# Performance work log

Measured on AMD Instinct MI355X. Metric: run time of the kernel, lower is better.

## Reference

```python
import jax, jax.numpy as jnp
import numpy as np

B, S, N, BS, D, H, V = 1, 2048, 128, 16, 512, 8, 32000
MASK_TOKEN_ID = 3


def setup_inputs() -> dict:
    key = jax.random.key(0)
    ks = jax.random.split(key, 10)
    anchors = jnp.sort(jax.random.randint(ks[0], (B, N), 0, S - BS), axis=1)
    return {
        "input_ids": jax.random.randint(ks[1], (B, S), 0, V),
        "hidden_states": jax.random.normal(ks[2], (B, S, D), dtype=jnp.float32),
        "loss_mask": jnp.ones((B, S), dtype=jnp.float32),
        "anchor_positions": anchors,
        "block_keep_mask": jnp.ones((B, N), dtype=bool),
        "embed_table": jax.random.normal(ks[3], (V, D), dtype=jnp.float32) * 0.02,
        "Wq": jax.random.normal(ks[4], (D, D), dtype=jnp.float32) * 0.02,
        "Wk": jax.random.normal(ks[5], (D, D), dtype=jnp.float32) * 0.02,
        "Wv": jax.random.normal(ks[6], (D, D), dtype=jnp.float32) * 0.02,
        "Wo": jax.random.normal(ks[7], (D, D), dtype=jnp.float32) * 0.02,
        "W_lm": jax.random.normal(ks[8], (D, V), dtype=jnp.float32) * 0.02,
    }


def dflash_sdpa_mask(anchor_positions, block_keep_mask):
    # KV layout: [context S | block_0 .. block_{N-1}], Q layout: [block_0 .. block_{N-1}]
    Q = N * BS
    KV = S + N * BS
    q_idx = jnp.arange(Q)              # [Q]
    kv_idx = jnp.arange(KV)            # [KV]
    q_blk = q_idx // BS                # [Q]
    anchor_q = anchor_positions[:, q_blk]          # [B,Q] anchor of each query's block
    keep_q = block_keep_mask[:, q_blk]             # [B,Q]
    is_ctx = kv_idx < S                             # [KV]
    mask_context = is_ctx[None, None, :] & (kv_idx[None, None, :] < anchor_q[:, :, None])  # [B,Q,KV]
    kv_blk = (kv_idx - S) // BS
    mask_draft = (kv_idx >= S)[None, :] & (q_blk[:, None] == kv_blk[None, :])              # [Q,KV]
    final = (mask_context | mask_draft[None]) & keep_q[:, :, None]                          # [B,Q,KV]
    return final


def reference(input_ids, hidden_states, loss_mask, anchor_positions, block_keep_mask,
              embed_table, Wq, Wk, Wv, Wo, W_lm):
    dh = D // H
    Q = N * BS

    # --- noise embedding: MASK token everywhere, anchor token at each block start ---
    safe_anchor = jnp.clip(anchor_positions, 0, S - 1)                     # [B,N]
    anchor_tokens = jnp.take_along_axis(input_ids, safe_anchor, axis=1)    # [B,N]
    start_tokens = jnp.where(block_keep_mask, anchor_tokens, MASK_TOKEN_ID)
    noise_ids = jnp.full((B, Q), MASK_TOKEN_ID, dtype=input_ids.dtype)
    noise_ids = noise_ids.at[:, jnp.arange(N) * BS].set(start_tokens)
    noise_embedding = embed_table[noise_ids]                               # [B,Q,D]

    # --- draft attention: Q = draft tokens, KV = [context hiddens | draft tokens] ---
    kv_in = jnp.concatenate([hidden_states, noise_embedding], axis=1)      # [B,S+Q,D]
    q = (noise_embedding @ Wq).reshape(B, Q, H, dh)
    k = (kv_in @ Wk).reshape(B, S + Q, H, dh)
    v = (kv_in @ Wv).reshape(B, S + Q, H, dh)
    scores = jnp.einsum("bqhd,bkhd->bhqk", q, k) / jnp.sqrt(jnp.float32(dh))
    mask = dflash_sdpa_mask(anchor_positions, block_keep_mask)[:, None]    # [B,1,Q,KV]
    attn = jax.nn.softmax(jnp.where(mask, scores, -1e9), axis=-1)
    out = jnp.einsum("bhqk,bkhd->bqhd", attn, v).reshape(B, Q, D) @ Wo     # [B,Q,D]
    logits = out @ W_lm                                                    # [B,Q,V]

    # --- block-wise CE loss ---
    offs = jnp.arange(BS)
    label_idx = anchor_positions[:, :, None] + offs[None, None, :]         # [B,N,BS]
    valid_label = label_idx < S
    safe_idx = jnp.clip(label_idx, 0, S - 1)
    ids_b = jnp.broadcast_to(input_ids[:, None, :], (B, N, S))
    target_ids = jnp.take_along_axis(ids_b, safe_idx, axis=2)              # [B,N,BS]
    lm_b = jnp.broadcast_to(loss_mask[:, None, :], (B, N, S))
    lm_g = jnp.take_along_axis(lm_b, safe_idx, axis=2)
    weight = (block_keep_mask[:, :, None].astype(jnp.float32)
              * valid_label.astype(jnp.float32)
              * (offs > 0)[None, None, :].astype(jnp.float32)
              * lm_g)                                                      # [B,N,BS]

    flat_logits = logits.reshape(-1, V)
    flat_targets = target_ids.reshape(-1)
    flat_w = weight.reshape(-1)
    logp = jax.nn.log_softmax(flat_logits, axis=-1)
    loss_per = -jnp.take_along_axis(logp, flat_targets[:, None], axis=1)[:, 0]
    loss = jnp.sum(loss_per * flat_w) / (jnp.sum(flat_w) + 1e-6)

    pred = jnp.argmax(flat_logits, axis=-1)
    correct = (pred == flat_targets) & (flat_w > 0.5)
    accuracy = jnp.sum(correct).astype(jnp.float32) / (jnp.sum(flat_w) + 1e-6)
    return loss, accuracy
```

## Files before the change

### kernel.cpp

```cpp
#include <hip/hip_runtime.h>

typedef unsigned short u16;
typedef __attribute__((ext_vector_type(4))) float f32x4;
typedef __attribute__((ext_vector_type(8))) short short8;
typedef __attribute__((ext_vector_type(4))) unsigned int uv4;
typedef __attribute__((ext_vector_type(4))) float fv4;
typedef __attribute__((ext_vector_type(4))) unsigned short usv4;

#define S_LEN 2048
#define NBLK 128
#define DMODEL 512
#define VOCAB 32000
#define QLEN 2048
#define KVLEN 4096
#define NSPLIT 250

#define GAS(p) ((const __attribute__((address_space(1))) void*)(const void*)(p))
#define LAS(p) ((__attribute__((address_space(3))) void*)(void*)(p))

__device__ __forceinline__ float bf2f(u16 u){
  union { unsigned int i; float f; } x; x.i = ((unsigned int)u) << 16; return x.f;
}
__device__ __forceinline__ u16 f2bf(float f){
  union { float f; unsigned int i; } x; x.f = f;
  unsigned int r = x.i + 0x7fffu + ((x.i >> 16) & 1u);
  return (u16)(r >> 16);
}

__global__ __launch_bounds__(256) void prep_w(const float* __restrict__ Wq, const float* __restrict__ Wk,
                                              const float* __restrict__ Wv, const float* __restrict__ Wo,
                                              const float* __restrict__ Wlm,
                                              u16* __restrict__ WqT, u16* __restrict__ WkT,
                                              u16* __restrict__ WvT, u16* __restrict__ WoT,
                                              u16* __restrict__ Wf){
  __shared__ float tile[64][33];
  int t = threadIdx.x;
  int id = blockIdx.x;
  if (id < 1024){
    const float* in; u16* out;
    switch (id >> 8){
      case 0: in = Wq; out = WqT; break;
      case 1: in = Wk; out = WkT; break;
      case 2: in = Wv; out = WvT; break;
      default: in = Wo; out = WoT; break;
    }
    int rem = id & 255;
    int nb = (rem & 15) * 32, kb = (rem >> 4) * 32;
    int tx = t & 31, ty = t >> 5;
    #pragma unroll
    for (int i = 0; i < 4; i++){
      int r = ty + i * 8;
      tile[r][tx] = in[(size_t)(kb + r) * 512 + nb + tx];
    }
    __syncthreads();
    #pragma unroll
    for (int i = 0; i < 4; i++){
      int r = ty + i * 8;
      out[(size_t)(nb + r) * 512 + kb + tx] = f2bf(tile[tx][r]);
    }
  } else {
    int j = id - 1024;
    int vb32 = j % 1000, kblk = j / 1000;
    int tx = t & 31, ty = t >> 5;
    #pragma unroll
    for (int i = 0; i < 8; i++){
      int r = ty + i * 8;
      tile[r][tx] = Wlm[(size_t)(kblk * 64 + r) * VOCAB + vb32 * 32 + tx];
    }
    __syncthreads();
    int w = t >> 6, lane = t & 63;
    int v16sel = w & 1, ktsel = w >> 1;
    int gsel = lane >> 4, li = lane & 15;
    u16 tmp[8];
    #pragma unroll
    for (int jj = 0; jj < 8; jj++)
      tmp[jj] = f2bf(tile[ktsel * 32 + gsel * 8 + jj][v16sel * 16 + li]);
    size_t v16 = vb32 * 2 + v16sel;
    size_t kt32 = kblk * 2 + ktsel;
    *(uv4*)&Wf[((v16 * 16 + kt32) * 64 + lane) * 8] = *(uv4*)tmp;
  }
}

__global__ __launch_bounds__(128) void build_kv(const float* __restrict__ hidden,
                                                const float* __restrict__ embed,
                                                const int* __restrict__ input_ids,
                                                const int* __restrict__ anchors,
                                                const unsigned char* __restrict__ keep,
                                                u16* __restrict__ kvb){
  int row = blockIdx.x;
  int t = threadIdx.x;
  const float* src;
  if (row < S_LEN){
    src = hidden + (size_t)row * DMODEL;
  } else {
    int q = row - S_LEN;
    int id = 3;
    if ((q & 15) == 0){
      int n = q >> 4;
      if (keep[n]){
        int a = anchors[n]; a = min(max(a, 0), S_LEN - 1);
        id = input_ids[a];
      }
    }
    src = embed + (size_t)id * DMODEL;
  }
  int c = t * 4;
  fv4 v = *(const fv4*)&src[c];
  usv4 o; o[0] = f2bf(v[0]); o[1] = f2bf(v[1]); o[2] = f2bf(v[2]); o[3] = f2bf(v[3]);
  *(usv4*)&kvb[(size_t)row * DMODEL + c] = o;
}

__global__ __launch_bounds__(256) void qkv_gemm(const u16* __restrict__ kvb,
                                                const u16* __restrict__ WkT,
                                                const u16* __restrict__ WvT,
                                                const u16* __restrict__ WqT,
                                                u16* __restrict__ kb,
                                                u16* __restrict__ vTb,
                                                u16* __restrict__ qb2){
  __shared__ __align__(16) u16 As[2][128 * 64];
  __shared__ __align__(16) u16 Bs[2][64 * 64];
  int id = blockIdx.x;
  const u16* A = kvb; const u16* BT; u16* C; int ldc; int trans = 0;
  int rowbase, colbase;
  if (id < 256){
    BT = WkT; C = kb; ldc = 512;
    rowbase = (id & 31) * 128; colbase = (id >> 5) * 64;
  } else if (id < 512){
    int j = id - 256;
    BT = WvT; C = vTb; ldc = KVLEN; trans = 1;
    rowbase = (j & 31) * 128; colbase = (j >> 5) * 64;
  } else {
    int j = id - 512;
    A = kvb + (size_t)S_LEN * DMODEL;
    BT = WqT; C = qb2; ldc = 512;
    rowbase = (j & 15) * 128; colbase = (j >> 4) * 64;
  }
  int t = threadIdx.x, w = t >> 6, lane = t & 63;
  int g = lane >> 4, li = lane & 15;
  int r0 = t >> 3, cg0 = t & 7;
  int swz = (cg0 ^ (r0 & 7)) << 3;

  auto stageA = [&](u16* dst, int kb_){
    #pragma unroll
    for (int i = 0; i < 4; i++)
      __builtin_amdgcn_global_load_lds(GAS(&A[(size_t)(rowbase + r0 + i * 32) * DMODEL + kb_ + swz]),
                                       LAS(dst + i * 2048 + w * 512), 16, 0, 0);
  };
  auto stageB = [&](u16* dst, int kb_){
    #pragma unroll
    for (int i = 0; i < 2; i++)
      __builtin_amdgcn_global_load_lds(GAS(&BT[(size_t)(colbase + r0 + i * 32) * DMODEL + kb_ + swz]),
                                       LAS(dst + i * 2048 + w * 512), 16, 0, 0);
  };

  f32x4 acc[2][4];
  #pragma unroll
  for (int i = 0; i < 2; i++)
    #pragma unroll
    for (int j = 0; j < 4; j++)
      acc[i][j] = (f32x4){0.f, 0.f, 0.f, 0.f};

  stageA(As[0], 0); stageB(Bs[0], 0);

  for (int kt = 0; kt < 8; kt++){
    u16* curA = As[kt & 1]; u16* curB = Bs[kt & 1];
    if (kt < 7){
      stageA(As[(kt + 1) & 1], (kt + 1) * 64); stageB(Bs[(kt + 1) & 1], (kt + 1) * 64);
      asm volatile("s_waitcnt vmcnt(6)" ::: "memory");
    } else {
      asm volatile("s_waitcnt vmcnt(0)" ::: "memory");
    }
    __builtin_amdgcn_s_barrier();
    #pragma unroll
    for (int ks = 0; ks < 2; ks++){
      short8 af[2], bf[4];
      #pragma unroll
      for (int mf = 0; mf < 2; mf++){
        int row = w * 32 + mf * 16 + li;
        af[mf] = *(const short8*)&curA[row * 64 + (((ks * 4 + g) ^ (li & 7)) << 3)];
      }
      #pragma unroll
      for (int nf = 0; nf < 4; nf++){
        int row = nf * 16 + li;
        bf[nf] = *(const short8*)&curB[row * 64 + (((ks * 4 + g) ^ (li & 7)) << 3)];
      }
      #pragma unroll
      for (int mf = 0; mf < 2; mf++)
        #pragma unroll
        for (int nf = 0; nf < 4; nf++)
          acc[mf][nf] = __builtin_amdgcn_mfma_f32_16x16x32_bf16(af[mf], bf[nf], acc[mf][nf], 0, 0, 0);
    }
    __builtin_amdgcn_s_barrier();
  }

  #pragma unroll
  for (int mf = 0; mf < 2; mf++)
    #pragma unroll
    for (int nf = 0; nf < 4; nf++)
      #pragma unroll
      for (int r = 0; r < 4; r++){
        int row = rowbase + w * 32 + mf * 16 + g * 4 + r;
        int col = colbase + nf * 16 + li;
        u16 vv = f2bf(acc[mf][nf][r]);
        if (trans) C[(size_t)col * ldc + row] = vv;
        else       C[(size_t)row * ldc + col] = vv;
      }
}

__global__ __launch_bounds__(256) void gemmO(const u16* __restrict__ A,
                                             const u16* __restrict__ BT,
                                             u16* __restrict__ C){
  __shared__ __align__(16) u16 As[2][128 * 64];
  __shared__ __align__(16) u16 Bs[2][64 * 64];
  int t = threadIdx.x, w = t >> 6, lane = t & 63;
  int g = lane >> 4, li = lane & 15;
  int rowbase = blockIdx.x * 128, colbase = blockIdx.y * 64;
  int r0 = t >> 3, cg0 = t & 7;
  int swz = (cg0 ^ (r0 & 7)) << 3;

  auto stageA = [&](u16* dst, int kb_){
    #pragma unroll
    for (int i = 0; i < 4; i++)
      __builtin_amdgcn_global_load_lds(GAS(&A[(size_t)(rowbase + r0 + i * 32) * DMODEL + kb_ + swz]),
                                       LAS(dst + i * 2048 + w * 512), 16, 0, 0);
  };
  auto stageB = [&](u16* dst, int kb_){
    #pragma unroll
    for (int i = 0; i < 2; i++)
      __builtin_amdgcn_global_load_lds(GAS(&BT[(size_t)(colbase + r0 + i * 32) * DMODEL + kb_ + swz]),
                                       LAS(dst + i * 2048 + w * 512), 16, 0, 0);
  };

  f32x4 acc[2][4];
  #pragma unroll
  for (int i = 0; i < 2; i++)
    #pragma unroll
    for (int j = 0; j < 4; j++)
      acc[i][j] = (f32x4){0.f, 0.f, 0.f, 0.f};

  stageA(As[0], 0); stageB(Bs[0], 0);

  for (int kt = 0; kt < 8; kt++){
    u16* curA = As[kt & 1]; u16* curB = Bs[kt & 1];
    if (kt < 7){
      stageA(As[(kt + 1) & 1], (kt + 1) * 64); stageB(Bs[(kt + 1) & 1], (kt + 1) * 64);
      asm volatile("s_waitcnt vmcnt(6)" ::: "memory");
    } else {
      asm volatile("s_waitcnt vmcnt(0)" ::: "memory");
    }
    __builtin_amdgcn_s_barrier();
    #pragma unroll
    for (int ks = 0; ks < 2; ks++){
      short8 af[2], bf[4];
      #pragma unroll
      for (int mf = 0; mf < 2; mf++){
        int row = w * 32 + mf * 16 + li;
        af[mf] = *(const short8*)&curA[row * 64 + (((ks * 4 + g) ^ (li & 7)) << 3)];
      }
      #pragma unroll
      for (int nf = 0; nf < 4; nf++){
        int row = nf * 16 + li;
        bf[nf] = *(const short8*)&curB[row * 64 + (((ks * 4 + g) ^ (li & 7)) << 3)];
      }
      #pragma unroll
      for (int mf = 0; mf < 2; mf++)
        #pragma unroll
        for (int nf = 0; nf < 4; nf++)
          acc[mf][nf] = __builtin_amdgcn_mfma_f32_16x16x32_bf16(af[mf], bf[nf], acc[mf][nf], 0, 0, 0);
    }
    __builtin_amdgcn_s_barrier();
  }

  #pragma unroll
  for (int mf = 0; mf < 2; mf++)
    #pragma unroll
    for (int nf = 0; nf < 4; nf++)
      #pragma unroll
      for (int r = 0; r < 4; r++){
        int row = rowbase + w * 32 + mf * 16 + g * 4 + r;
        int col = colbase + nf * 16 + li;
        C[(size_t)row * DMODEL + col] = f2bf(acc[mf][nf][r]);
      }
}

__global__ __launch_bounds__(256) void attn_mfma(const u16* __restrict__ qb,
                                                 const u16* __restrict__ kb,
                                                 const u16* __restrict__ vT,
                                                 const int* __restrict__ anchors,
                                                 const unsigned char* __restrict__ keep,
                                                 u16* __restrict__ attnb){
  int bx = blockIdx.x;
  int n = (bx & 1) ? (NBLK - 1 - (bx >> 1)) : (bx >> 1);
  int h = blockIdx.y;
  int t = threadIdx.x, w = t >> 6, lane = t & 63;
  int g = lane >> 4, li = lane & 15;

  __shared__ __align__(16) u16 q_s[16][72];
  __shared__ __align__(16) u16 p_s[4][16][72];
  __shared__ float o_s[4][16][64];
  __shared__ float l_s[4][16];

  {
    int r = t >> 4, c4 = (t & 15) * 4;
    usv4 v = *(const usv4*)&qb[(size_t)(n * 16 + r) * DMODEL + h * 64 + c4];
    usv4 o;
    #pragma unroll
    for (int j = 0; j < 4; j++) o[j] = f2bf(bf2f(v[j]) * 0.125f);
    *(usv4*)&q_s[r][c4] = o;
  }
  __syncthreads();

  int anchor = anchors[n];
  bool kp = keep[n] != 0;
  const u16* kh  = kb + h * 64;
  const u16* vTh = vT + (size_t)(h * 64) * KVLEN;

  if (!kp){
    if (w == 0){
      float acc = 0.f;
      const u16* row = vTh + (size_t)lane * KVLEN;
      for (int k2 = 0; k2 < KVLEN; k2 += 8){
        short8 vv = *(const short8*)&row[k2];
        #pragma unroll
        for (int j = 0; j < 8; j++) acc += bf2f((u16)vv[j]);
      }
      acc *= (1.f / 4096.f);
      u16 ov = f2bf(acc);
      for (int r = 0; r < 16; r++)
        attnb[(size_t)(n * 16 + r) * DMODEL + h * 64 + lane] = ov;
    }
    return;
  }

  short8 qa[2];
  #pragma unroll
  for (int ks = 0; ks < 2; ks++)
    qa[ks] = *(const short8*)&q_s[li][ks * 32 + g * 8];

  int nctx = (anchor + 63) >> 6;
  int ntot = nctx + 1;

  f32x4 o_acc[4];
  float l[4];
  #pragma unroll
  for (int i = 0; i < 4; i++){ o_acc[i] = (f32x4){0.f,0.f,0.f,0.f}; l[i] = 0.f; }

  for (int c = w; c < ntot; c += 4){
    bool draft = (c == nctx);
    int kbase = draft ? (S_LEN + n * 16) : c * 64;
    int nk    = draft ? 16 : min(64, anchor - c * 64);

    f32x4 s[4];
    #pragma unroll
    for (int nf = 0; nf < 4; nf++) s[nf] = (f32x4){0.f,0.f,0.f,0.f};
    #pragma unroll
    for (int ks = 0; ks < 2; ks++){
      #pragma unroll
      for (int nf = 0; nf < 4; nf++){
        int krow = min(kbase + nf * 16 + li, KVLEN - 1);
        short8 bfrag = *(const short8*)&kh[(size_t)krow * DMODEL + ks * 32 + g * 8];
        s[nf] = __builtin_amdgcn_mfma_f32_16x16x32_bf16(qa[ks], bfrag, s[nf], 0, 0, 0);
      }
    }

    #pragma unroll
    for (int r = 0; r < 4; r++){
      float ps = 0.f;
      #pragma unroll
      for (int nf = 0; nf < 4; nf++){
        float p = (nf * 16 + li < nk) ? __expf(s[nf][r]) : 0.f;
        ps += p;
        p_s[w][g * 4 + r][nf * 16 + li] = f2bf(p);
      }
      #pragma unroll
      for (int mm = 1; mm < 16; mm <<= 1) ps += __shfl_xor(ps, mm);
      l[r] += ps;
    }

    #pragma unroll
    for (int ks = 0; ks < 2; ks++){
      short8 pa = *(const short8*)&p_s[w][li][ks * 32 + g * 8];
      int kcol = min(kbase + ks * 32 + g * 8, KVLEN - 8);
      #pragma unroll
      for (int nfd = 0; nfd < 4; nfd++){
        short8 vfrag = *(const short8*)&vTh[(size_t)(nfd * 16 + li) * KVLEN + kcol];
        o_acc[nfd] = __builtin_amdgcn_mfma_f32_16x16x32_bf16(pa, vfrag, o_acc[nfd], 0, 0, 0);
      }
    }
  }

  #pragma unroll
  for (int r = 0; r < 4; r++){
    if (li == 0) l_s[w][g * 4 + r] = l[r];
    #pragma unroll
    for (int nfd = 0; nfd < 4; nfd++)
      o_s[w][g * 4 + r][nfd * 16 + li] = o_acc[nfd][r];
  }
  __syncthreads();

  {
    int row = t >> 4, c0 = (t & 15) * 4;
    float L = l_s[0][row] + l_s[1][row] + l_s[2][row] + l_s[3][row];
    float inv = 1.f / L;
    #pragma unroll
    for (int j = 0; j < 4; j++){
      float ov = o_s[0][row][c0 + j] + o_s[1][row][c0 + j] + o_s[2][row][c0 + j] + o_s[3][row][c0 + j];
      attnb[(size_t)(n * 16 + row) * DMODEL + h * 64 + c0 + j] = f2bf(ov * inv);
    }
  }
}

__global__ __launch_bounds__(256) void lm_fused(const u16* __restrict__ obp,
                                                const u16* __restrict__ Wf,
                                                const int* __restrict__ input_ids,
                                                const int* __restrict__ anchors,
                                                float* __restrict__ pl,
                                                float* __restrict__ pt, float* __restrict__ pbv,
                                                int* __restrict__ pbi){
  __shared__ __align__(16) u16 Ob[2][128 * 64];
  __shared__ int tcol_s[128];

  int L = blockIdx.x;
  int T = (L & 7) * 500 + (L >> 3);
  int qbase = (T & 15) * 128;
  int vb = T >> 4;
  int vocabbase = vb * 128;
  int t = threadIdx.x, w = t >> 6, lane = t & 63;
  int g = lane >> 4, li = lane & 15;
  int wv = w & 1, wq = w >> 1;

  if (t < 128){
    int r = qbase + t; int n = r >> 4, off = r & 15;
    int lab = anchors[n] + off;
    int safe = min(max(lab, 0), S_LEN - 1);
    tcol_s[t] = input_ids[safe];
  }

  int r0 = t >> 3, cg0 = t & 7;
  int swz = (cg0 ^ (r0 & 7)) << 3;
  auto stageO = [&](u16* odst, int kt){
    #pragma unroll
    for (int i = 0; i < 4; i++)
      __builtin_amdgcn_global_load_lds(GAS(&obp[(size_t)(qbase + r0 + i * 32) * DMODEL + kt * 64 + swz]),
                                       LAS(odst + i * 2048 + w * 512), 16, 0, 0);
  };
  const u16* wbase = Wf + ((size_t)(vb * 8 + wv * 4) * 16) * 512 + lane * 8;

  f32x4 acc[4][4];
  #pragma unroll
  for (int i = 0; i < 4; i++)
    #pragma unroll
    for (int j = 0; j < 4; j++)
      acc[i][j] = (f32x4){0.f, 0.f, 0.f, 0.f};

  stageO(Ob[0], 0);

  for (int kt = 0; kt < 8; kt++){
    const u16* curO = Ob[kt & 1];
    short8 wfr[2][4];
    if (kt < 7){
      stageO(Ob[(kt + 1) & 1], kt + 1);
      #pragma unroll
      for (int ks = 0; ks < 2; ks++)
        #pragma unroll
        for (int vf = 0; vf < 4; vf++)
          wfr[ks][vf] = *(const short8*)(wbase + ((size_t)(vf * 16 + kt * 2 + ks) * 64) * 8);
      asm volatile("s_waitcnt vmcnt(12)" ::: "memory");
    } else {
      #pragma unroll
      for (int ks = 0; ks < 2; ks++)
        #pragma unroll
        for (int vf = 0; vf < 4; vf++)
          wfr[ks][vf] = *(const short8*)(wbase + ((size_t)(vf * 16 + kt * 2 + ks) * 64) * 8);
      asm volatile("s_waitcnt vmcnt(8)" ::: "memory");
    }
    __builtin_amdgcn_s_barrier();
    __builtin_amdgcn_s_setprio(1);
    #pragma unroll
    for (int ks = 0; ks < 2; ks++){
      short8 obf[4];
      #pragma unroll
      for (int qf = 0; qf < 4; qf++)
        obf[qf] = *(const short8*)&curO[(wq * 64 + qf * 16 + li) * 64 + (((ks * 4 + g) ^ (li & 7)) << 3)];
      #pragma unroll
      for (int vf = 0; vf < 4; vf++)
        #pragma unroll
        for (int qf = 0; qf < 4; qf++)
          acc[vf][qf] = __builtin_amdgcn_mfma_f32_16x16x32_bf16(wfr[ks][vf], obf[qf], acc[vf][qf], 0, 0, 0);
    }
    __builtin_amdgcn_s_setprio(0);
    __builtin_amdgcn_s_barrier();
  }
  __syncthreads();

  float* cse = (float*)&Ob[0][0];
  float* ctv = (float*)&Ob[0][512];
  float* cbv = (float*)&Ob[0][1024];
  int*   cbi = (int*)  &Ob[0][1536];

  #pragma unroll
  for (int qf = 0; qf < 4; qf++){
    int qloc = wq * 64 + qf * 16 + li;
    int tc = tcol_s[qloc] - (vocabbase + wv * 64);
    float se = 0.f, tv = -3e38f, bv = -3e38f; int bi = 0x7fffffff;
    #pragma unroll
    for (int vf = 0; vf < 4; vf++){
      #pragma unroll
      for (int r = 0; r < 4; r++){
        float v = acc[vf][qf][r];
        int pos = vf * 16 + g * 4 + r;
        se += __expf(v);
        if (pos == tc) tv = v;
        if (v > bv){ bv = v; bi = pos; }
      }
    }
    #pragma unroll
    for (int off = 16; off <= 32; off <<= 1){
      se += __shfl_xor(se, off);
      tv = fmaxf(tv, __shfl_xor(tv, off));
      float ob_ = __shfl_xor(bv, off); int oi = __shfl_xor(bi, off);
      if (ob_ > bv || (ob_ == bv && oi < bi)){ bv = ob_; bi = oi; }
    }
    if (g == 0){
      cse[wv * 128 + qloc] = se; ctv[wv * 128 + qloc] = tv;
      cbv[wv * 128 + qloc] = bv; cbi[wv * 128 + qloc] = wv * 64 + bi;
    }
  }
  __syncthreads();

  if (t < 128){
    float SE = 0.f, TV = -3e38f, BV = -3e38f; int BI = 0x7fffffff;
    #pragma unroll
    for (int vv = 0; vv < 2; vv++){
      SE += cse[vv * 128 + t];
      TV = fmaxf(TV, ctv[vv * 128 + t]);
      float v = cbv[vv * 128 + t];
      if (v > BV){ BV = v; BI = cbi[vv * 128 + t]; }
    }
    size_t idx = (size_t)vb * QLEN + qbase + t;
    pl[idx] = SE; pt[idx] = TV; pbv[idx] = BV; pbi[idx] = vocabbase + BI;
  }
}

__global__ __launch_bounds__(256) void loss_rows(const float* __restrict__ pl,
                                                 const float* __restrict__ pt, const float* __restrict__ pbv,
                                                 const int* __restrict__ pbi,
                                                 const int* __restrict__ input_ids,
                                                 const int* __restrict__ anchors,
                                                 const unsigned char* __restrict__ keep,
                                                 const float* __restrict__ loss_mask,
                                                 float* __restrict__ rowacc){
  int t = threadIdx.x, w = t >> 6, lane = t & 63;
  int row = blockIdx.x * 4 + w;
  float L = 0.f, TV = -3e38f, BV = -3e38f; int BI = 0x7fffffff;
  for (int s = lane; s < NSPLIT; s += 64){
    size_t idx = (size_t)s * QLEN + row;
    L += pl[idx];
    TV = fmaxf(TV, pt[idx]);
    float bv_ = pbv[idx]; int bi_ = pbi[idx];
    if (bv_ > BV || (bv_ == BV && bi_ < BI)){ BV = bv_; BI = bi_; }
  }
  #pragma unroll
  for (int mm = 1; mm < 64; mm <<= 1){
    L += __shfl_xor(L, mm);
    TV = fmaxf(TV, __shfl_xor(TV, mm));
    float ob = __shfl_xor(BV, mm); int oi = __shfl_xor(BI, mm);
    if (ob > BV || (ob == BV && oi < BI)){ BV = ob; BI = oi; }
  }
  if (lane == 0){
    int n = row >> 4, off = row & 15;
    int lab = anchors[n] + off;
    int valid = (lab < S_LEN) ? 1 : 0;
    int safe = min(max(lab, 0), S_LEN - 1);
    int tgt = input_ids[safe];
    float wgt = (keep[n] ? 1.f : 0.f) * (valid ? 1.f : 0.f) * ((off > 0) ? 1.f : 0.f) * loss_mask[safe];
    float logp = TV - __logf(L);
    rowacc[row * 3 + 0] = -logp * wgt;
    rowacc[row * 3 + 1] = wgt;
    rowacc[row * 3 + 2] = ((BI == tgt) && (wgt > 0.5f)) ? 1.f : 0.f;
  }
}

__global__ __launch_bounds__(256) void final_sum(const float* __restrict__ rowacc, float* __restrict__ out){
  int t = threadIdx.x;
  float a = 0.f, b = 0.f, c = 0.f;
  for (int r = t; r < QLEN; r += 256){
    a += rowacc[r * 3 + 0]; b += rowacc[r * 3 + 1]; c += rowacc[r * 3 + 2];
  }
  __shared__ float sa[256], sb[256], sc_[256];
  sa[t] = a; sb[t] = b; sc_[t] = c;
  __syncthreads();
  for (int s = 128; s >= 1; s >>= 1){
    if (t < s){ sa[t] += sa[t + s]; sb[t] += sb[t + s]; sc_[t] += sc_[t + s]; }
    __syncthreads();
  }
  if (t == 0){
    out[0] = sa[0] / (sb[0] + 1e-6f);
    out[1] = sc_[0] / (sb[0] + 1e-6f);
  }
}

extern "C" void kernel_launch(void* const* d_in, const int* in_sizes, int n_in,
                              void* d_out, int out_size, void* d_ws, size_t ws_size,
                              hipStream_t stream) {
  const int*   input_ids = (const int*)  d_in[0];
  const float* hidden    = (const float*)d_in[1];
  const float* loss_mask = (const float*)d_in[2];
  const int*   anchors   = (const int*)  d_in[3];
  const unsigned char* keep = (const unsigned char*)d_in[4];
  const float* embed     = (const float*)d_in[5];
  const float* Wq        = (const float*)d_in[6];
  const float* Wk        = (const float*)d_in[7];
  const float* Wv        = (const float*)d_in[8];
  const float* Wo        = (const float*)d_in[9];
  const float* Wlm       = (const float*)d_in[10];

  char* ws = (char*)d_ws;
  size_t off = 0;
  auto take = [&](size_t bytes) -> char* {
    char* p = ws + off;
    off += (bytes + 255) & ~(size_t)255;
    return p;
  };
  u16* WqT  = (u16*)take((size_t)512 * 512 * 2);
  u16* WkT  = (u16*)take((size_t)512 * 512 * 2);
  u16* WvT  = (u16*)take((size_t)512 * 512 * 2);
  u16* WoT  = (u16*)take((size_t)512 * 512 * 2);
  u16* Wfrag= (u16*)take((size_t)VOCAB * 512 * 2);
  u16* kvb  = (u16*)take((size_t)KVLEN * 512 * 2);
  u16* qb2  = (u16*)take((size_t)QLEN * 512 * 2);
  u16* kb   = (u16*)take((size_t)KVLEN * 512 * 2);
  u16* vTb  = (u16*)take((size_t)512 * KVLEN * 2);
  u16* attnb= (u16*)take((size_t)QLEN * 512 * 2);
  u16* ob   = (u16*)take((size_t)QLEN * 512 * 2);
  float* pl = (float*)take((size_t)QLEN * NSPLIT * 4);
  float* pt = (float*)take((size_t)QLEN * NSPLIT * 4);
  float* pbv= (float*)take((size_t)QLEN * NSPLIT * 4);
  int*   pbi= (int*)  take((size_t)QLEN * NSPLIT * 4);
  float* rowacc = (float*)take((size_t)QLEN * 3 * 4);

  prep_w<<<9024, 256, 0, stream>>>(Wq, Wk, Wv, Wo, Wlm, WqT, WkT, WvT, WoT, Wfrag);

  build_kv<<<KVLEN, 128, 0, stream>>>(hidden, embed, input_ids, anchors, keep, kvb);

  qkv_gemm<<<640, 256, 0, stream>>>(kvb, WkT, WvT, WqT, kb, vTb, qb2);

  attn_mfma<<<dim3(NBLK, 8), 256, 0, stream>>>(qb2, kb, vTb, anchors, keep, attnb);

  gemmO<<<dim3(16, 8), 256, 0, stream>>>(attnb, WoT, ob);

  lm_fused<<<4000, 256, 0, stream>>>(ob, Wfrag, input_ids, anchors, pl, pt, pbv, pbi);

  loss_rows<<<512, 256, 0, stream>>>(pl, pt, pbv, pbi, input_ids, anchors, keep, loss_mask, rowacc);

  final_sum<<<1, 256, 0, stream>>>(rowacc, (float*)d_out);
}
```

Measured before the change: 200.8 us.

## Merge KV build into weight prep, shrink gemmO tiles, defer softmax row-sum reduction

Folds the build_kv work into the weight-prep kernel as extra blocks (two rows per 256-thread block), which removes one kernel launch. gemmO moves from 128-row to 64-row tiles, doubling the grid from 128 to 256 blocks so more CUs are busy on this small GEMM. The attention kernel now keeps per-lane partial sums of the softmax denominator and does the cross-lane shuffle reduction once after the loop instead of on every chunk. The cost is that each gemmO block reuses its B tile for fewer rows.

```diff
diff --git a/kernel.cpp b/kernel.cpp
--- a/kernel.cpp
+++ b/kernel.cpp
@@ -27,12 +27,18 @@
   return (u16)(r >> 16);
 }
 
-__global__ __launch_bounds__(256) void prep_w(const float* __restrict__ Wq, const float* __restrict__ Wk,
-                                              const float* __restrict__ Wv, const float* __restrict__ Wo,
-                                              const float* __restrict__ Wlm,
-                                              u16* __restrict__ WqT, u16* __restrict__ WkT,
-                                              u16* __restrict__ WvT, u16* __restrict__ WoT,
-                                              u16* __restrict__ Wf){
+__global__ __launch_bounds__(256) void prep_all(const float* __restrict__ Wq, const float* __restrict__ Wk,
+                                                const float* __restrict__ Wv, const float* __restrict__ Wo,
+                                                const float* __restrict__ Wlm,
+                                                const float* __restrict__ hidden,
+                                                const float* __restrict__ embed,
+                                                const int* __restrict__ input_ids,
+                                                const int* __restrict__ anchors,
+                                                const unsigned char* __restrict__ keep,
+                                                u16* __restrict__ WqT, u16* __restrict__ WkT,
+                                                u16* __restrict__ WvT, u16* __restrict__ WoT,
+                                                u16* __restrict__ Wf,
+                                                u16* __restrict__ kvb){
   __shared__ float tile[64][33];
   int t = threadIdx.x;
   int id = blockIdx.x;
@@ -58,7 +64,7 @@
       int r = ty + i * 8;
       out[(size_t)(nb + r) * 512 + kb + tx] = f2bf(tile[tx][r]);
     }
-  } else {
+  } else if (id < 9024){
     int j = id - 1024;
     int vb32 = j % 1000, kblk = j / 1000;
     int tx = t & 31, ty = t >> 5;
@@ -78,36 +84,30 @@
     size_t v16 = vb32 * 2 + v16sel;
     size_t kt32 = kblk * 2 + ktsel;
     *(uv4*)&Wf[((v16 * 16 + kt32) * 64 + lane) * 8] = *(uv4*)tmp;
-  }
-}
-
-__global__ __launch_bounds__(128) void build_kv(const float* __restrict__ hidden,
-                                                const float* __restrict__ embed,
-                                                const int* __restrict__ input_ids,
-                                                const int* __restrict__ anchors,
-                                                const unsigned char* __restrict__ keep,
-                                                u16* __restrict__ kvb){
-  int row = blockIdx.x;
-  int t = threadIdx.x;
-  const float* src;
-  if (row < S_LEN){
-    src = hidden + (size_t)row * DMODEL;
   } else {
-    int q = row - S_LEN;
-    int id = 3;
-    if ((q & 15) == 0){
-      int n = q >> 4;
-      if (keep[n]){
-        int a = anchors[n]; a = min(max(a, 0), S_LEN - 1);
-        id = input_ids[a];
-      }
-    }
-    src = embed + (size_t)id * DMODEL;
-  }
-  int c = t * 4;
-  fv4 v = *(const fv4*)&src[c];
-  usv4 o; o[0] = f2bf(v[0]); o[1] = f2bf(v[1]); o[2] = f2bf(v[2]); o[3] = f2bf(v[3]);
-  *(usv4*)&kvb[(size_t)row * DMODEL + c] = o;
+    int j2 = id - 9024;
+    int row = j2 * 2 + (t >> 7);
+    int tl = t & 127;
+    const float* src;
+    if (row < S_LEN){
+      src = hidden + (size_t)row * DMODEL;
+    } else {
+      int q = row - S_LEN;
+      int tok = 3;
+      if ((q & 15) == 0){
+        int n = q >> 4;
+        if (keep[n]){
+          int a = anchors[n]; a = min(max(a, 0), S_LEN - 1);
+          tok = input_ids[a];
+        }
+      }
+      src = embed + (size_t)tok * DMODEL;
+    }
+    int c = tl * 4;
+    fv4 v = *(const fv4*)&src[c];
+    usv4 o; o[0] = f2bf(v[0]); o[1] = f2bf(v[1]); o[2] = f2bf(v[2]); o[3] = f2bf(v[3]);
+    *(usv4*)&kvb[(size_t)row * DMODEL + c] = o;
+  }
 }
 
 __global__ __launch_bounds__(256) void qkv_gemm(const u16* __restrict__ kvb,
@@ -210,17 +210,17 @@
 __global__ __launch_bounds__(256) void gemmO(const u16* __restrict__ A,
                                              const u16* __restrict__ BT,
                                              u16* __restrict__ C){
-  __shared__ __align__(16) u16 As[2][128 * 64];
+  __shared__ __align__(16) u16 As[2][64 * 64];
   __shared__ __align__(16) u16 Bs[2][64 * 64];
   int t = threadIdx.x, w = t >> 6, lane = t & 63;
   int g = lane >> 4, li = lane & 15;
-  int rowbase = blockIdx.x * 128, colbase = blockIdx.y * 64;
+  int rowbase = blockIdx.x * 64, colbase = blockIdx.y * 64;
   int r0 = t >> 3, cg0 = t & 7;
   int swz = (cg0 ^ (r0 & 7)) << 3;
 
   auto stageA = [&](u16* dst, int kb_){
     #pragma unroll
-    for (int i = 0; i < 4; i++)
+    for (int i = 0; i < 2; i++)
       __builtin_amdgcn_global_load_lds(GAS(&A[(size_t)(rowbase + r0 + i * 32) * DMODEL + kb_ + swz]),
                                        LAS(dst + i * 2048 + w * 512), 16, 0, 0);
   };
@@ -231,12 +231,9 @@
                                        LAS(dst + i * 2048 + w * 512), 16, 0, 0);
   };
 
-  f32x4 acc[2][4];
-  #pragma unroll
-  for (int i = 0; i < 2; i++)
-    #pragma unroll
-    for (int j = 0; j < 4; j++)
-      acc[i][j] = (f32x4){0.f, 0.f, 0.f, 0.f};
+  f32x4 acc[4];
+  #pragma unroll
+  for (int j = 0; j < 4; j++) acc[j] = (f32x4){0.f, 0.f, 0.f, 0.f};
 
   stageA(As[0], 0); stageB(Bs[0], 0);
 
@@ -244,43 +241,39 @@
     u16* curA = As[kt & 1]; u16* curB = Bs[kt & 1];
     if (kt < 7){
       stageA(As[(kt + 1) & 1], (kt + 1) * 64); stageB(Bs[(kt + 1) & 1], (kt + 1) * 64);
-      asm volatile("s_waitcnt vmcnt(6)" ::: "memory");
+      asm volatile("s_waitcnt vmcnt(4)" ::: "memory");
     } else {
       asm volatile("s_waitcnt vmcnt(0)" ::: "memory");
     }
     __builtin_amdgcn_s_barrier();
     #pragma unroll
     for (int ks = 0; ks < 2; ks++){
-      short8 af[2], bf[4];
-      #pragma unroll
-      for (int mf = 0; mf < 2; mf++){
-        int row = w * 32 + mf * 16 + li;
-        af[mf] = *(const short8*)&curA[row * 64 + (((ks * 4 + g) ^ (li & 7)) << 3)];
-      }
+      short8 af;
+      {
+        int row = w * 16 + li;
+        af = *(const short8*)&curA[row * 64 + (((ks * 4 + g) ^ (li & 7)) << 3)];
+      }
+      short8 bf[4];
       #pragma unroll
       for (int nf = 0; nf < 4; nf++){
         int row = nf * 16 + li;
         bf[nf] = *(const short8*)&curB[row * 64 + (((ks * 4 + g) ^ (li & 7)) << 3)];
       }
       #pragma unroll
-      for (int mf = 0; mf < 2; mf++)
-        #pragma unroll
-        for (int nf = 0; nf < 4; nf++)
-          acc[mf][nf] = __builtin_amdgcn_mfma_f32_16x16x32_bf16(af[mf], bf[nf], acc[mf][nf], 0, 0, 0);
+      for (int nf = 0; nf < 4; nf++)
+        acc[nf] = __builtin_amdgcn_mfma_f32_16x16x32_bf16(af, bf[nf], acc[nf], 0, 0, 0);
     }
     __builtin_amdgcn_s_barrier();
   }
 
   #pragma unroll
-  for (int mf = 0; mf < 2; mf++)
-    #pragma unroll
-    for (int nf = 0; nf < 4; nf++)
-      #pragma unroll
-      for (int r = 0; r < 4; r++){
-        int row = rowbase + w * 32 + mf * 16 + g * 4 + r;
-        int col = colbase + nf * 16 + li;
-        C[(size_t)row * DMODEL + col] = f2bf(acc[mf][nf][r]);
-      }
+  for (int nf = 0; nf < 4; nf++)
+    #pragma unroll
+    for (int r = 0; r < 4; r++){
+      int row = rowbase + w * 16 + g * 4 + r;
+      int col = colbase + nf * 16 + li;
+      C[(size_t)row * DMODEL + col] = f2bf(acc[nf][r]);
+    }
 }
 
 __global__ __launch_bounds__(256) void attn_mfma(const u16* __restrict__ qb,
@@ -341,9 +334,9 @@
   int ntot = nctx + 1;
 
   f32x4 o_acc[4];
-  float l[4];
-  #pragma unroll
-  for (int i = 0; i < 4; i++){ o_acc[i] = (f32x4){0.f,0.f,0.f,0.f}; l[i] = 0.f; }
+  float lp[4];
+  #pragma unroll
+  for (int i = 0; i < 4; i++){ o_acc[i] = (f32x4){0.f,0.f,0.f,0.f}; lp[i] = 0.f; }
 
   for (int c = w; c < ntot; c += 4){
     bool draft = (c == nctx);
@@ -365,16 +358,12 @@
 
     #pragma unroll
     for (int r = 0; r < 4; r++){
-      float ps = 0.f;
       #pragma unroll
       for (int nf = 0; nf < 4; nf++){
         float p = (nf * 16 + li < nk) ? __expf(s[nf][r]) : 0.f;
-        ps += p;
+        lp[r] += p;
         p_s[w][g * 4 + r][nf * 16 + li] = f2bf(p);
       }
-      #pragma unroll
-      for (int mm = 1; mm < 16; mm <<= 1) ps += __shfl_xor(ps, mm);
-      l[r] += ps;
     }
 
     #pragma unroll
@@ -391,7 +380,10 @@
 
   #pragma unroll
   for (int r = 0; r < 4; r++){
-    if (li == 0) l_s[w][g * 4 + r] = l[r];
+    float ps = lp[r];
+    #pragma unroll
+    for (int mm = 1; mm < 16; mm <<= 1) ps += __shfl_xor(ps, mm);
+    if (li == 0) l_s[w][g * 4 + r] = ps;
     #pragma unroll
     for (int nfd = 0; nfd < 4; nfd++)
       o_s[w][g * 4 + r][nfd * 16 + li] = o_acc[nfd][r];
@@ -639,15 +631,14 @@
   int*   pbi= (int*)  take((size_t)QLEN * NSPLIT * 4);
   float* rowacc = (float*)take((size_t)QLEN * 3 * 4);
 
-  prep_w<<<9024, 256, 0, stream>>>(Wq, Wk, Wv, Wo, Wlm, WqT, WkT, WvT, WoT, Wfrag);
-
-  build_kv<<<KVLEN, 128, 0, stream>>>(hidden, embed, input_ids, anchors, keep, kvb);
+  prep_all<<<11072, 256, 0, stream>>>(Wq, Wk, Wv, Wo, Wlm, hidden, embed, input_ids, anchors, keep,
+                                      WqT, WkT, WvT, WoT, Wfrag, kvb);
 
   qkv_gemm<<<640, 256, 0, stream>>>(kvb, WkT, WvT, WqT, kb, vTb, qb2);
 
   attn_mfma<<<dim3(NBLK, 8), 256, 0, stream>>>(qb2, kb, vTb, anchors, keep, attnb);
 
-  gemmO<<<dim3(16, 8), 256, 0, stream>>>(attnb, WoT, ob);
+  gemmO<<<dim3(32, 8), 256, 0, stream>>>(attnb, WoT, ob);
 
   lm_fused<<<4000, 256, 0, stream>>>(ob, Wfrag, input_ids, anchors, pl, pt, pbv, pbi);
 
```

After: 195.8 us, median of 2. -2.5%, faster.
